# Performance work log

Measured on AMD Instinct MI355X. Metric: run time of the kernel, lower is better.

## Reference

```python
import jax, jax.numpy as jnp
import numpy as np

BSZ, LEN, DIN, DOUT = 16, 2048, 256, 256
DENSITY = 0.05

def setup_inputs() -> dict:
    key = jax.random.key(0)
    k1, k2, k3 = jax.random.split(key, 3)
    x = jax.random.normal(k1, (BSZ, LEN, DIN), dtype=jnp.float32)
    # binary symmetric adjacency, zero diagonal (self-loops added inside GCN)
    m = jax.random.uniform(k2, (LEN, LEN)) < DENSITY
    g = jnp.maximum(m, m.T).astype(jnp.float32) * (1.0 - jnp.eye(LEN, dtype=jnp.float32))
    graph = g[None]  # module squeezes leading dim
    W = (jax.random.normal(k3, (DIN, DOUT), dtype=jnp.float32) / np.sqrt(DIN)).astype(jnp.float32)
    b = jnp.zeros((DOUT,), dtype=jnp.float32)
    return {"x": x, "graph": graph, "W": W, "b": b}

def reference(x, graph, W, b):
    # x: [B, L, Din]; graph: [1, L, L] binary adjacency (shared across batch)
    B, L, _ = x.shape
    A = graph[0] + jnp.eye(L, dtype=x.dtype)           # add self-loops (GCNConv default)
    deg = A.sum(axis=0)                                # degree incl. self-loop (unit edge weights)
    dinv = jnp.where(deg > 0, jax.lax.rsqrt(deg), 0.0)
    An = dinv[:, None] * A * dinv[None, :]             # D^-1/2 (A+I) D^-1/2, symmetric
    h = jnp.einsum('bld,do->blo', x, W)                # dense linear transform
    agg = jnp.einsum('ml,bmo->blo', An, h) + b         # out[l] = sum_m norm[m,l] * h[m]
    return jax.nn.relu(agg) + x                        # relu + residual
```

## Files before the change

### kernel.cpp

```cpp
#include <hip/hip_runtime.h>
#include <hip/hip_bf16.h>
#include <stdint.h>

#define LL 2048
#define NB 16
#define DD 256
#define NT2 16

typedef __bf16 bf16x8 __attribute__((ext_vector_type(8)));
typedef float f32x4 __attribute__((ext_vector_type(4)));
typedef int i32x4 __attribute__((ext_vector_type(4)));
typedef int i32x8 __attribute__((ext_vector_type(8)));
union Frag8 { i32x8 v8; i32x4 v4[2]; };

__device__ __forceinline__ unsigned short f2bf(float f) {
    uint32_t u = __float_as_uint(f);
    u = (u + 0x7FFFu + ((u >> 16) & 1u)) >> 16;
    return (unsigned short)u;
}

__device__ __forceinline__ float bf2f(unsigned short v) {
    return __uint_as_float(((uint32_t)v) << 16);
}

#if __has_builtin(__builtin_amdgcn_cvt_pk_fp8_f32)
__device__ __forceinline__ uint32_t pk4fp8(float a, float b, float c, float d) {
    int r = 0;
    r = __builtin_amdgcn_cvt_pk_fp8_f32(a, b, r, false);
    r = __builtin_amdgcn_cvt_pk_fp8_f32(c, d, r, true);
    return (uint32_t)r;
}
#else
__device__ __forceinline__ uint32_t f2fp8_1(float f) {
    uint32_t u = __float_as_uint(f);
    uint32_t s = (u >> 24) & 0x80u;
    uint32_t au = u & 0x7FFFFFFFu;
    float af = __uint_as_float(au);
    if (af >= 448.0f) return s | 0x7Eu;
    if (af < 0x1p-6f) {
        uint32_t q = (uint32_t)rintf(af * 512.0f);
        return s | q;
    }
    uint32_t r = au + (0x7FFFFu + ((au >> 20) & 1u));
    uint32_t e8 = (r >> 23) - 120u;
    return s | (e8 << 3) | ((r >> 20) & 7u);
}
__device__ __forceinline__ uint32_t pk4fp8(float a, float b, float c, float d) {
    return f2fp8_1(a) | (f2fp8_1(b) << 8) | (f2fp8_1(c) << 16) | (f2fp8_1(d) << 24);
}
#endif

__device__ __forceinline__ float fp8tof(uint32_t b) {
    uint32_t s = (b & 0x80u) << 24;
    uint32_t e = (b >> 3) & 15u, m = b & 7u;
    float v = (e == 0) ? (float)m * 0x1p-9f
            : __uint_as_float(((e + 120u) << 23) | (m << 20));
    return __uint_as_float(__float_as_uint(v) | s);
}

__device__ __forceinline__ void gload16(const void* g, void* l) {
    __builtin_amdgcn_global_load_lds(
        (const __attribute__((address_space(1))) void*)g,
        (__attribute__((address_space(3))) void*)l,
        16, 0, 0);
}

#define DSREAD(dst, off) asm volatile("ds_read_b128 %0, %1" : "=v"(dst) : "v"(off))

__global__ __launch_bounds__(256) void prep_graph(
        const float* __restrict__ graph, float* __restrict__ dinv,
        uint8_t* __restrict__ gq) {
    int r = blockIdx.x;
    int t = threadIdx.x;
    const float4* row = (const float4*)(graph + (size_t)r * LL);
    float4 v0 = row[t * 2 + 0];
    float4 v1 = row[t * 2 + 1];
    float s = v0.x + v0.y + v0.z + v0.w + v1.x + v1.y + v1.z + v1.w;

    uint32_t lo = (v0.x != 0.f ? 0x38u : 0u) | ((v0.y != 0.f ? 0x38u : 0u) << 8)
                | ((v0.z != 0.f ? 0x38u : 0u) << 16) | ((v0.w != 0.f ? 0x38u : 0u) << 24);
    uint32_t hi = (v1.x != 0.f ? 0x38u : 0u) | ((v1.y != 0.f ? 0x38u : 0u) << 8)
                | ((v1.z != 0.f ? 0x38u : 0u) << 16) | ((v1.w != 0.f ? 0x38u : 0u) << 24);
    *(uint2*)(gq + (size_t)r * LL + t * 8) = make_uint2(lo, hi);

    #pragma unroll
    for (int off = 32; off > 0; off >>= 1) s += __shfl_down(s, off, 64);
    __shared__ float red[4];
    if ((t & 63) == 0) red[t >> 6] = s;
    __syncthreads();
    if (t == 0) {
        float deg = red[0] + red[1] + red[2] + red[3] + 1.0f;
        dinv[r] = 1.0f / sqrtf(deg);
    }
}

__global__ __launch_bounds__(256) void prep_w(
        const float* __restrict__ W, unsigned short* __restrict__ Wt) {
    int tid = blockIdx.x * 256 + threadIdx.x;
    int d = tid >> 8, o = tid & 255;
    Wt[o * DD + d] = f2bf(W[tid]);
}

__global__ __launch_bounds__(256) void linear_kernel(
        const float* __restrict__ x, const unsigned short* __restrict__ Wt,
        const float* __restrict__ dinv, uint8_t* __restrict__ Pq) {
    __shared__ __align__(16) unsigned short Al[128][64];
    __shared__ __align__(16) unsigned short Bl[128][64];
    int t = threadIdx.x;
    int w = t >> 6, ln = t & 63;
    int m0 = blockIdx.x * 128;
    int n0 = blockIdx.y * 128;
    int b  = m0 >> 11;
    int ml0 = m0 & (LL - 1);
    int wm = w >> 1, wn = w & 1;
    int lr = ln & 15, lg = ln >> 4;

    f32x4 acc[4][4] = {};

    for (int k0 = 0; k0 < DD; k0 += 64) {
        #pragma unroll
        for (int it = 0; it < 8; ++it) {
            int c = it * 256 + t;
            int row = c >> 4, col = (c & 15) * 4;
            float4 v = *(const float4*)(x + (size_t)(m0 + row) * DD + k0 + col);
            *(ushort4*)(&Al[row][col]) =
                make_ushort4(f2bf(v.x), f2bf(v.y), f2bf(v.z), f2bf(v.w));
        }
        #pragma unroll
        for (int it = 0; it < 4; ++it) {
            int c = it * 256 + t;
            const unsigned short* g = Wt + (size_t)(n0 + (c >> 3)) * DD + k0 + (c & 7) * 8;
            unsigned short* lp = &Bl[0][0] + (size_t)(it * 256 + w * 64) * 8;
            gload16(g, lp);
        }
        __syncthreads();
        #pragma unroll
        for (int kk = 0; kk < 64; kk += 32) {
            bf16x8 af[4], bq[4];
            #pragma unroll
            for (int i = 0; i < 4; ++i)
                af[i] = *(const bf16x8*)&Al[wm * 64 + i * 16 + lr][kk + lg * 8];
            #pragma unroll
            for (int j = 0; j < 4; ++j)
                bq[j] = *(const bf16x8*)&Bl[wn * 64 + j * 16 + lr][kk + lg * 8];
            #pragma unroll
            for (int i = 0; i < 4; ++i)
                #pragma unroll
                for (int j = 0; j < 4; ++j)
                    acc[i][j] = __builtin_amdgcn_mfma_f32_16x16x32_bf16(
                        af[i], bq[j], acc[i][j], 0, 0, 0);
        }
        __syncthreads();
    }

    #pragma unroll
    for (int i = 0; i < 4; ++i) {
        int ml = ml0 + wm * 64 + i * 16 + lg * 4;
        float4 dv = *(const float4*)(dinv + ml);
        #pragma unroll
        for (int j = 0; j < 4; ++j) {
            int o = n0 + wn * 64 + j * 16 + lr;
            uint32_t pk = pk4fp8(dv.x * acc[i][j][0], dv.y * acc[i][j][1],
                                 dv.z * acc[i][j][2], dv.w * acc[i][j][3]);
            *(uint32_t*)(Pq + ((size_t)(b * DD + o)) * LL + ml) = pk;
        }
    }
}

__global__ __launch_bounds__(512, 2) void agg_kernel(
        const uint8_t* __restrict__ gq, const uint8_t* __restrict__ Pq,
        const float* __restrict__ dinv, const float* __restrict__ bias,
        const float* __restrict__ x, float* __restrict__ out) {
    __shared__ unsigned char lds[3 * 49152];

    const int t = threadIdx.x;
    const int w = t >> 6, ln = t & 63;
    const int wm = w >> 2, wn = w & 3;
    const int lr = ln & 15, lg = ln >> 4;
    const int s7 = lr & 7;

    int bid = blockIdx.x;
    int wg = (bid & 7) * 32 + (bid >> 3);
    const int l0 = (wg & 15) * 128;
    const int n0 = (wg >> 4) * 256;

    const int rt = t >> 3;
    const int st = (t & 7) ^ (rt & 7);
    const uint8_t* a0 = gq + (size_t)(l0 + rt) * LL + st * 16;
    const uint8_t* a1 = a0 + (size_t)64 * LL;
    const uint8_t* b0 = Pq + (size_t)(n0 + rt) * LL + st * 16;
    const uint8_t* b1 = b0 + (size_t)64 * LL;
    const uint8_t* b2 = b0 + (size_t)128 * LL;
    const uint8_t* b3 = b0 + (size_t)192 * LL;
    const int wd = w * 1024;

    f32x4 acc[4][4] = {};

    #pragma unroll
    for (int kt = 0; kt < 2; ++kt) {
        int sbp = kt * 49152, ko = kt * 128;
        gload16(a0 + ko, lds + sbp + wd);
        gload16(a1 + ko, lds + sbp + 8192 + wd);
        gload16(b0 + ko, lds + sbp + 16384 + wd);
        gload16(b1 + ko, lds + sbp + 24576 + wd);
        gload16(b2 + ko, lds + sbp + 32768 + wd);
        gload16(b3 + ko, lds + sbp + 40960 + wd);
    }
    asm volatile("s_waitcnt vmcnt(6)" ::: "memory");
    __builtin_amdgcn_s_barrier();

    int cur = 0;
    for (int it = 0; it < NT2; ++it) {
        int stg = cur - 1; if (stg < 0) stg = 2;
        const int ktn = (it + 2 < NT2) ? it + 2 : NT2 - 1;
        const int cb = cur * 49152;
        const int sb = stg * 49152;
        const int ko = ktn * 128;

        Frag8 fb[4], fa[2];
        #pragma unroll
        for (int j = 0; j < 4; ++j)
            #pragma unroll
            for (int h = 0; h < 2; ++h) {
                int off = cb + 16384 + (wn * 64 + j * 16 + lr) * 128
                        + (((lg * 2 + h) ^ s7) << 4);
                DSREAD(fb[j].v4[h], off);
            }
        #pragma unroll
        for (int i = 0; i < 2; ++i)
            #pragma unroll
            for (int h = 0; h < 2; ++h) {
                int off = cb + (wm * 64 + i * 16 + lr) * 128
                        + (((lg * 2 + h) ^ s7) << 4);
                DSREAD(fa[i].v4[h], off);
            }
        gload16(a0 + ko, lds + sb + wd);
        gload16(a1 + ko, lds + sb + 8192 + wd);
        gload16(b0 + ko, lds + sb + 16384 + wd);
        __builtin_amdgcn_s_barrier();
        asm volatile("s_waitcnt lgkmcnt(0)" ::: "memory");
        __builtin_amdgcn_sched_barrier(0);
        __builtin_amdgcn_s_setprio(1);
        #pragma unroll
        for (int i = 0; i < 2; ++i)
            #pragma unroll
            for (int j = 0; j < 4; ++j)
                acc[i][j] = __builtin_amdgcn_mfma_scale_f32_16x16x128_f8f6f4(
                    fa[i].v8, fb[j].v8, acc[i][j], 0, 0, 0, 127, 0, 127);
        __builtin_amdgcn_s_setprio(0);
        __builtin_amdgcn_sched_barrier(0);
        __builtin_amdgcn_s_barrier();

        Frag8 fc[2];
        #pragma unroll
        for (int i = 0; i < 2; ++i)
            #pragma unroll
            for (int h = 0; h < 2; ++h) {
                int off = cb + (wm * 64 + (i + 2) * 16 + lr) * 128
                        + (((lg * 2 + h) ^ s7) << 4);
                DSREAD(fc[i].v4[h], off);
            }
        gload16(b1 + ko, lds + sb + 24576 + wd);
        gload16(b2 + ko, lds + sb + 32768 + wd);
        gload16(b3 + ko, lds + sb + 40960 + wd);
        __builtin_amdgcn_s_barrier();
        asm volatile("s_waitcnt lgkmcnt(0)" ::: "memory");
        __builtin_amdgcn_sched_barrier(0);
        __builtin_amdgcn_s_setprio(1);
        #pragma unroll
        for (int i = 0; i < 2; ++i)
            #pragma unroll
            for (int j = 0; j < 4; ++j)
                acc[i + 2][j] = __builtin_amdgcn_mfma_scale_f32_16x16x128_f8f6f4(
                    fc[i].v8, fb[j].v8, acc[i + 2][j], 0, 0, 0, 127, 0, 127);
        __builtin_amdgcn_s_setprio(0);
        __builtin_amdgcn_sched_barrier(0);
        asm volatile("s_waitcnt vmcnt(6)" ::: "memory");
        __builtin_amdgcn_s_barrier();

        cur = (cur == 2) ? 0 : cur + 1;
    }

    const int b = n0 >> 8;
    #pragma unroll
    for (int j = 0; j < 4; ++j) {
        int np = n0 + wn * 64 + j * 16 + lr;
        int o = np & (DD - 1);
        float bo = bias[o];
        #pragma unroll
        for (int i = 0; i < 4; ++i) {
            int lrow = l0 + wm * 64 + i * 16 + lg * 4;
            float4 dv = *(const float4*)(dinv + lrow);
            uchar4 pv = *(const uchar4*)(Pq + (size_t)np * LL + lrow);
            float dva[4] = {dv.x, dv.y, dv.z, dv.w};
            float pva[4] = {fp8tof(pv.x), fp8tof(pv.y), fp8tof(pv.z), fp8tof(pv.w)};
            #pragma unroll
            for (int r = 0; r < 4; ++r) {
                float aggv = dva[r] * (acc[i][j][r] + pva[r]) + bo;
                float rl = fmaxf(aggv, 0.0f);
                size_t oi = ((size_t)(b * LL + lrow + r)) * DD + o;
                out[oi] = rl + x[oi];
            }
        }
    }
}

extern "C" void kernel_launch(void* const* d_in, const int* in_sizes, int n_in,
                              void* d_out, int out_size, void* d_ws, size_t ws_size,
                              hipStream_t stream) {
    const float* x     = (const float*)d_in[0];
    const float* graph = (const float*)d_in[1];
    const float* W     = (const float*)d_in[2];
    const float* bias  = (const float*)d_in[3];
    float* out = (float*)d_out;

    char* ws = (char*)d_ws;
    float*          dinv = (float*)ws;
    uint8_t*        gq   = (uint8_t*)(ws + 8192);
    unsigned short* Wt   = (unsigned short*)(ws + 8192 + 4194304);
    uint8_t*        Pq   = (uint8_t*)(ws + 8192 + 4194304 + 131072);

    prep_graph<<<LL, 256, 0, stream>>>(graph, dinv, gq);
    prep_w<<<DD, 256, 0, stream>>>(W, Wt);
    linear_kernel<<<dim3((NB * LL) / 128, DD / 128), 256, 0, stream>>>(x, Wt, dinv, Pq);
    agg_kernel<<<256, 512, 0, stream>>>(gq, Pq, dinv, bias, x, out);
}
```

Before: 63.35 us.

## Shrink aggregation tile to 128x128 with 4 waves and double buffering

```diff
diff --git a/kernel.cpp b/kernel.cpp
--- a/kernel.cpp
+++ b/kernel.cpp
@@ -14,9 +14,8 @@
 union Frag8 { i32x8 v8; i32x4 v4[2]; };
 
 __device__ __forceinline__ unsigned short f2bf(float f) {
-    uint32_t u = __float_as_uint(f);
-    u = (u + 0x7FFFu + ((u >> 16) & 1u)) >> 16;
-    return (unsigned short)u;
+    __hip_bfloat16 h = __float2bfloat16(f);
+    return *reinterpret_cast<unsigned short*>(&h);
 }
 
 __device__ __forceinline__ float bf2f(unsigned short v) {
@@ -167,57 +166,61 @@
     }
 }
 
-__global__ __launch_bounds__(512, 2) void agg_kernel(
+__global__ __launch_bounds__(256, 2) void agg_kernel(
         const uint8_t* __restrict__ gq, const uint8_t* __restrict__ Pq,
         const float* __restrict__ dinv, const float* __restrict__ bias,
         const float* __restrict__ x, float* __restrict__ out) {
-    __shared__ unsigned char lds[3 * 49152];
+    __shared__ unsigned char lds[2 * 32768];
 
     const int t = threadIdx.x;
     const int w = t >> 6, ln = t & 63;
-    const int wm = w >> 2, wn = w & 3;
+    const int wm = w >> 1, wn = w & 1;
     const int lr = ln & 15, lg = ln >> 4;
     const int s7 = lr & 7;
 
     int bid = blockIdx.x;
-    int wg = (bid & 7) * 32 + (bid >> 3);
+    int wg = (bid & 7) * 64 + (bid >> 3);
     const int l0 = (wg & 15) * 128;
-    const int n0 = (wg >> 4) * 256;
-
-    const int rt = t >> 3;
-    const int st = (t & 7) ^ (rt & 7);
-    const uint8_t* a0 = gq + (size_t)(l0 + rt) * LL + st * 16;
-    const uint8_t* a1 = a0 + (size_t)64 * LL;
-    const uint8_t* b0 = Pq + (size_t)(n0 + rt) * LL + st * 16;
-    const uint8_t* b1 = b0 + (size_t)64 * LL;
-    const uint8_t* b2 = b0 + (size_t)128 * LL;
-    const uint8_t* b3 = b0 + (size_t)192 * LL;
+    const int n0 = (wg >> 4) * 128;
+
+    const int rt8 = t >> 3;
+    const int st = (t & 7) ^ (rt8 & 7);
+    const uint8_t* ag = gq + (size_t)(l0 + rt8) * LL + st * 16;
+    const uint8_t* bg = Pq + (size_t)(n0 + rt8) * LL + st * 16;
     const int wd = w * 1024;
 
     f32x4 acc[4][4] = {};
 
     #pragma unroll
-    for (int kt = 0; kt < 2; ++kt) {
-        int sbp = kt * 49152, ko = kt * 128;
-        gload16(a0 + ko, lds + sbp + wd);
-        gload16(a1 + ko, lds + sbp + 8192 + wd);
-        gload16(b0 + ko, lds + sbp + 16384 + wd);
-        gload16(b1 + ko, lds + sbp + 24576 + wd);
-        gload16(b2 + ko, lds + sbp + 32768 + wd);
-        gload16(b3 + ko, lds + sbp + 40960 + wd);
-    }
-    asm volatile("s_waitcnt vmcnt(6)" ::: "memory");
+    for (int r = 0; r < 4; ++r) {
+        gload16(ag + (size_t)(32 * r) * LL, lds + r * 4096 + wd);
+        gload16(bg + (size_t)(32 * r) * LL, lds + 16384 + r * 4096 + wd);
+    }
+    asm volatile("s_waitcnt vmcnt(0)" ::: "memory");
     __builtin_amdgcn_s_barrier();
 
-    int cur = 0;
     for (int it = 0; it < NT2; ++it) {
-        int stg = cur - 1; if (stg < 0) stg = 2;
-        const int ktn = (it + 2 < NT2) ? it + 2 : NT2 - 1;
-        const int cb = cur * 49152;
-        const int sb = stg * 49152;
-        const int ko = ktn * 128;
-
-        Frag8 fb[4], fa[2];
+        const int cb = (it & 1) * 32768;
+        const int sb = cb ^ 32768;
+
+        if (it + 1 < NT2) {
+            const int ko = (it + 1) * 128;
+            #pragma unroll
+            for (int r = 0; r < 4; ++r) {
+                gload16(ag + (size_t)(32 * r) * LL + ko, lds + sb + r * 4096 + wd);
+                gload16(bg + (size_t)(32 * r) * LL + ko, lds + sb + 16384 + r * 4096 + wd);
+            }
+        }
+
+        Frag8 fa[4], fb[4];
+        #pragma unroll
+        for (int i = 0; i < 4; ++i)
+            #pragma unroll
+            for (int h = 0; h < 2; ++h) {
+                int off = cb + (wm * 64 + i * 16 + lr) * 128
+                        + (((lg * 2 + h) ^ s7) << 4);
+                DSREAD(fa[i].v4[h], off);
+            }
         #pragma unroll
         for (int j = 0; j < 4; ++j)
             #pragma unroll
@@ -226,59 +229,19 @@
                         + (((lg * 2 + h) ^ s7) << 4);
                 DSREAD(fb[j].v4[h], off);
             }
-        #pragma unroll
-        for (int i = 0; i < 2; ++i)
-            #pragma unroll
-            for (int h = 0; h < 2; ++h) {
-                int off = cb + (wm * 64 + i * 16 + lr) * 128
-                        + (((lg * 2 + h) ^ s7) << 4);
-                DSREAD(fa[i].v4[h], off);
-            }
-        gload16(a0 + ko, lds + sb + wd);
-        gload16(a1 + ko, lds + sb + 8192 + wd);
-        gload16(b0 + ko, lds + sb + 16384 + wd);
-        __builtin_amdgcn_s_barrier();
         asm volatile("s_waitcnt lgkmcnt(0)" ::: "memory");
         __builtin_amdgcn_sched_barrier(0);
         __builtin_amdgcn_s_setprio(1);
         #pragma unroll
-        for (int i = 0; i < 2; ++i)
+        for (int i = 0; i < 4; ++i)
             #pragma unroll
             for (int j = 0; j < 4; ++j)
                 acc[i][j] = __builtin_amdgcn_mfma_scale_f32_16x16x128_f8f6f4(
                     fa[i].v8, fb[j].v8, acc[i][j], 0, 0, 0, 127, 0, 127);
         __builtin_amdgcn_s_setprio(0);
         __builtin_amdgcn_sched_barrier(0);
+        asm volatile("s_waitcnt vmcnt(0)" ::: "memory");
         __builtin_amdgcn_s_barrier();
-
-        Frag8 fc[2];
-        #pragma unroll
-        for (int i = 0; i < 2; ++i)
-            #pragma unroll
-            for (int h = 0; h < 2; ++h) {
-                int off = cb + (wm * 64 + (i + 2) * 16 + lr) * 128
-                        + (((lg * 2 + h) ^ s7) << 4);
-                DSREAD(fc[i].v4[h], off);
-            }
-        gload16(b1 + ko, lds + sb + 24576 + wd);
-        gload16(b2 + ko, lds + sb + 32768 + wd);
-        gload16(b3 + ko, lds + sb + 40960 + wd);
-        __builtin_amdgcn_s_barrier();
-        asm volatile("s_waitcnt lgkmcnt(0)" ::: "memory");
-        __builtin_amdgcn_sched_barrier(0);
-        __builtin_amdgcn_s_setprio(1);
-        #pragma unroll
-        for (int i = 0; i < 2; ++i)
-            #pragma unroll
-            for (int j = 0; j < 4; ++j)
-                acc[i + 2][j] = __builtin_amdgcn_mfma_scale_f32_16x16x128_f8f6f4(
-                    fc[i].v8, fb[j].v8, acc[i + 2][j], 0, 0, 0, 127, 0, 127);
-        __builtin_amdgcn_s_setprio(0);
-        __builtin_amdgcn_sched_barrier(0);
-        asm volatile("s_waitcnt vmcnt(6)" ::: "memory");
-        __builtin_amdgcn_s_barrier();
-
-        cur = (cur == 2) ? 0 : cur + 1;
     }
 
     const int b = n0 >> 8;
@@ -323,5 +286,5 @@
     prep_graph<<<LL, 256, 0, stream>>>(graph, dinv, gq);
     prep_w<<<DD, 256, 0, stream>>>(W, Wt);
     linear_kernel<<<dim3((NB * LL) / 128, DD / 128), 256, 0, stream>>>(x, Wt, dinv, Pq);
-    agg_kernel<<<256, 512, 0, stream>>>(gq, Pq, dinv, bias, x, out);
-}
+    agg_kernel<<<512, 256, 0, stream>>>(gq, Pq, dinv, bias, x, out);
+}
```

Measured after the change: 57.66 us. -9.0%, faster.
